# Performance work log

Hardware: AMD Instinct MI355X
Metric: run time of the kernel (lower is better)

## Reference

```python
import jax, jax.numpy as jnp
import numpy as np

P = 2048
IMG_H = IMG_W = 128
FOV = 1.0471975512  # 60 deg vertical/horizontal fov
ZNEAR, ZFAR = 0.01, 100.0
SH_C0 = 0.28209479177387814
LOWPASS = 0.3  # 3DGS low-pass filter added to 2D covariance diagonal


def _camera():
    view = np.eye(4, dtype=np.float32)
    view[2, 3] = 4.0  # camera at world z=-4 looking down +z
    tanf = np.tan(FOV / 2)
    pm = np.zeros((4, 4), dtype=np.float32)
    pm[0, 0] = 1.0 / tanf
    pm[1, 1] = 1.0 / tanf
    pm[2, 2] = ZFAR / (ZFAR - ZNEAR)
    pm[2, 3] = -ZFAR * ZNEAR / (ZFAR - ZNEAR)
    pm[3, 2] = 1.0
    proj = (pm @ view).astype(np.float32)
    campos = np.array([0.0, 0.0, -4.0], dtype=np.float32)
    return view, proj, campos


def setup_inputs() -> dict:
    key = jax.random.key(0)
    ks = jax.random.split(key, 6)
    view, proj, campos = _camera()
    return {
        'means_3d': jax.random.normal(ks[0], (P, 3), dtype=jnp.float32) * 0.8,
        'means_2d': jnp.zeros((P, 2), dtype=jnp.float32),
        'features': jax.random.uniform(ks[1], (P, 3), dtype=jnp.float32),
        'opacities': jax.random.uniform(ks[2], (P, 1), dtype=jnp.float32) * 0.9 + 0.05,
        'scales': jax.random.uniform(ks[3], (P, 3), dtype=jnp.float32) * 0.08 + 0.01,
        'rotations': jax.random.normal(ks[4], (P, 4), dtype=jnp.float32),
        'viewmatrix': jnp.asarray(view),
        'projmatrix': jnp.asarray(proj),
        'campos': jnp.asarray(campos),
        'image_height': IMG_H,
        'image_width': IMG_W,
    }


def _quat_to_rot(q):
    q = q / jnp.linalg.norm(q, axis=-1, keepdims=True)
    w, x, y, z = q[:, 0], q[:, 1], q[:, 2], q[:, 3]
    R = jnp.stack([
        1 - 2 * (y * y + z * z), 2 * (x * y - w * z), 2 * (x * z + w * y),
        2 * (x * y + w * z), 1 - 2 * (x * x + z * z), 2 * (y * z - w * x),
        2 * (x * z - w * y), 2 * (y * z + w * x), 1 - 2 * (x * x + y * y),
    ], axis=-1).reshape(-1, 3, 3)
    return R


def _rasterize(means_3d, features, opacities, scales, rotations, viewmatrix, projmatrix, H, W):
    tanf = jnp.tan(FOV / 2)
    focal_x = W / (2.0 * tanf)
    focal_y = H / (2.0 * tanf)

    # camera-space positions [P,3]
    t = means_3d @ viewmatrix[:3, :3].T + viewmatrix[:3, 3]
    depth = t[:, 2]

    # projected pixel centers (ndc2pix)
    ph = means_3d @ projmatrix[:3, :3].T + projmatrix[:3, 3]
    pw = means_3d @ projmatrix[3, :3] + projmatrix[3, 3]
    ndc = ph[:, :2] / (pw[:, None] + 1e-7)
    px = ((ndc[:, 0] + 1.0) * W - 1.0) * 0.5
    py = ((ndc[:, 1] + 1.0) * H - 1.0) * 0.5

    # 3D covariance: Sigma = R S S^T R^T
    Rm = _quat_to_rot(rotations)
    M = Rm * scales[:, None, :]  # R @ diag(s)
    sigma = M @ jnp.swapaxes(M, 1, 2)  # [P,3,3]

    # EWA splat: 2D covariance = J W Sigma W^T J^T
    lim = 1.3 * tanf
    tz = depth
    tx = jnp.clip(t[:, 0] / tz, -lim, lim) * tz
    ty = jnp.clip(t[:, 1] / tz, -lim, lim) * tz
    zeros = jnp.zeros_like(tz)
    J = jnp.stack([
        jnp.stack([focal_x / tz, zeros, -focal_x * tx / (tz * tz)], -1),
        jnp.stack([zeros, focal_y / tz, -focal_y * ty / (tz * tz)], -1),
    ], axis=1)  # [P,2,3]
    Tm = J @ viewmatrix[:3, :3]
    cov2d = Tm @ sigma @ jnp.swapaxes(Tm, 1, 2)  # [P,2,2]
    a = cov2d[:, 0, 0] + LOWPASS
    b = cov2d[:, 0, 1]
    c = cov2d[:, 1, 1] + LOWPASS
    det = a * c - b * b
    valid = (depth > 0.2) & (det > 0.0)
    det_s = jnp.where(valid, det, 1.0)
    conic_a, conic_b, conic_c = c / det_s, -b / det_s, a / det_s

    # radii from max eigenvalue
    mid = 0.5 * (a + c)
    lam = mid + jnp.sqrt(jnp.maximum(mid * mid - det, 0.1))
    radii = jnp.where(valid, jnp.ceil(3.0 * jnp.sqrt(lam)), 0.0)

    # SH degree-0 color
    color = jnp.maximum(SH_C0 * features + 0.5, 0.0)  # [P,3]

    # depth sort, front to back
    order = jnp.argsort(jnp.where(valid, depth, jnp.inf))
    px_s, py_s = px[order], py[order]
    ca, cb, cc = conic_a[order], conic_b[order], conic_c[order]
    op_s = opacities[order, 0]
    col_s = color[order]
    valid_s = valid[order]

    # pixel grid
    gx, gy = jnp.meshgrid(jnp.arange(W, dtype=jnp.float32), jnp.arange(H, dtype=jnp.float32))
    gx = gx.reshape(-1)
    gy = gy.reshape(-1)  # [HW]

    dx = gx[None, :] - px_s[:, None]  # [P,HW]
    dy = gy[None, :] - py_s[:, None]
    power = -0.5 * (ca[:, None] * dx * dx + cc[:, None] * dy * dy) - cb[:, None] * dx * dy
    alpha = jnp.minimum(0.99, op_s[:, None] * jnp.exp(jnp.minimum(power, 0.0)))
    skip = (power > 0.0) | (alpha < 1.0 / 255.0) | (~valid_s)[:, None]
    alpha = jnp.where(skip, 0.0, alpha)

    one_m = 1.0 - alpha
    incl = jnp.cumprod(one_m, axis=0)
    T_excl = jnp.concatenate([jnp.ones((1, H * W), dtype=alpha.dtype), incl[:-1]], axis=0)
    w = T_excl * alpha  # [P,HW]
    img = jnp.einsum('pn,pc->cn', w, col_s)  # [3,HW]
    T_final = incl[-1]
    img = img + T_final[None, :]  # bg_color = (1,1,1)
    return img.reshape(3, H, W), radii


def reference(means_3d, means_2d, features, opacities, scales, rotations, viewmatrix, projmatrix, campos, image_height, image_width):
    # means_2d and campos are interface placeholders (means_2d receives grads only
    # inside the CUDA kernel; campos only matters for sh_degree > 0)
    return _rasterize(means_3d, features, opacities, scales, rotations, viewmatrix, projmatrix, image_height, image_width)
```

## Files before the change

### kernel.cpp

```cpp
#include <hip/hip_runtime.h>
#include <math.h>


#define IMG 128
#define NPIX (IMG * IMG)
#define GS 12
#define SORT_N 2048

__device__ __forceinline__ void gproj(int i,
                                      const float* __restrict__ means,
                                      const float* __restrict__ rots,
                                      const float* __restrict__ scales,
                                      const float* __restrict__ vm,
                                      const float* __restrict__ pm,
                                      float& depth, bool& valid,
                                      float& px, float& py,
                                      float& ca, float& cb, float& cc,
                                      float& lam)
{
    const float W = (float)IMG, H = (float)IMG;
    const float tanfov = 0.5773502691896258f;
    const float focal_x = W / (2.0f * tanfov);
    const float focal_y = H / (2.0f * tanfov);
    const float lim = 1.3f * tanfov;

    float mx = means[3 * i + 0], my = means[3 * i + 1], mz = means[3 * i + 2];

    float tx = vm[0] * mx + vm[1] * my + vm[2]  * mz + vm[3];
    float ty = vm[4] * mx + vm[5] * my + vm[6]  * mz + vm[7];
    float tz = vm[8] * mx + vm[9] * my + vm[10] * mz + vm[11];
    depth = tz;

    float ph0 = pm[0]  * mx + pm[1]  * my + pm[2]  * mz + pm[3];
    float ph1 = pm[4]  * mx + pm[5]  * my + pm[6]  * mz + pm[7];
    float pw  = pm[12] * mx + pm[13] * my + pm[14] * mz + pm[15];
    float rinv = 1.0f / (pw + 1e-7f);
    px = ((ph0 * rinv + 1.0f) * W - 1.0f) * 0.5f;
    py = ((ph1 * rinv + 1.0f) * H - 1.0f) * 0.5f;

    float qw = rots[4 * i + 0], qx = rots[4 * i + 1], qy = rots[4 * i + 2], qz = rots[4 * i + 3];
    float qn = sqrtf(qw * qw + qx * qx + qy * qy + qz * qz);
    qw /= qn; qx /= qn; qy /= qn; qz /= qn;
    float R00 = 1.0f - 2.0f * (qy * qy + qz * qz), R01 = 2.0f * (qx * qy - qw * qz), R02 = 2.0f * (qx * qz + qw * qy);
    float R10 = 2.0f * (qx * qy + qw * qz), R11 = 1.0f - 2.0f * (qx * qx + qz * qz), R12 = 2.0f * (qy * qz - qw * qx);
    float R20 = 2.0f * (qx * qz - qw * qy), R21 = 2.0f * (qy * qz + qw * qx), R22 = 1.0f - 2.0f * (qx * qx + qy * qy);

    float sx = scales[3 * i + 0], sy = scales[3 * i + 1], sz = scales[3 * i + 2];
    float M00 = R00 * sx, M01 = R01 * sy, M02 = R02 * sz;
    float M10 = R10 * sx, M11 = R11 * sy, M12 = R12 * sz;
    float M20 = R20 * sx, M21 = R21 * sy, M22 = R22 * sz;
    float S00 = M00 * M00 + M01 * M01 + M02 * M02;
    float S01 = M00 * M10 + M01 * M11 + M02 * M12;
    float S02 = M00 * M20 + M01 * M21 + M02 * M22;
    float S11 = M10 * M10 + M11 * M11 + M12 * M12;
    float S12 = M10 * M20 + M11 * M21 + M12 * M22;
    float S22 = M20 * M20 + M21 * M21 + M22 * M22;

    float txc = fminf(fmaxf(tx / tz, -lim), lim) * tz;
    float tyc = fminf(fmaxf(ty / tz, -lim), lim) * tz;
    float J00 = focal_x / tz, J02 = -focal_x * txc / (tz * tz);
    float J11 = focal_y / tz, J12 = -focal_y * tyc / (tz * tz);

    float T00 = J00 * vm[0] + J02 * vm[8];
    float T01 = J00 * vm[1] + J02 * vm[9];
    float T02 = J00 * vm[2] + J02 * vm[10];
    float T10 = J11 * vm[4] + J12 * vm[8];
    float T11 = J11 * vm[5] + J12 * vm[9];
    float T12 = J11 * vm[6] + J12 * vm[10];

    float U00 = T00 * S00 + T01 * S01 + T02 * S02;
    float U01 = T00 * S01 + T01 * S11 + T02 * S12;
    float U02 = T00 * S02 + T01 * S12 + T02 * S22;
    float U10 = T10 * S00 + T11 * S01 + T12 * S02;
    float U11 = T10 * S01 + T11 * S11 + T12 * S12;
    float U12 = T10 * S02 + T11 * S12 + T12 * S22;
    float C00 = U00 * T00 + U01 * T01 + U02 * T02;
    float C01 = U00 * T10 + U01 * T11 + U02 * T12;
    float C11 = U10 * T10 + U11 * T11 + U12 * T12;

    float a = C00 + 0.3f, b = C01, c = C11 + 0.3f;
    float det = a * c - b * b;
    valid = (depth > 0.2f) && (det > 0.0f);
    float det_s = valid ? det : 1.0f;
    ca = c / det_s; cb = -b / det_s; cc = a / det_s;

    float mid = 0.5f * (a + c);
    lam = mid + sqrtf(fmaxf(mid * mid - det, 0.1f));
}

__global__ void gsplat_prep_rank_scatter(const float* __restrict__ means,
                                         const float* __restrict__ feats,
                                         const float* __restrict__ ops,
                                         const float* __restrict__ scales,
                                         const float* __restrict__ rots,
                                         const float* __restrict__ vm,
                                         const float* __restrict__ pm,
                                         float* __restrict__ gS,
                                         float4* __restrict__ culls,
                                         float* __restrict__ radii_out,
                                         int P)
{
    __shared__ unsigned int sk[SORT_N];
    __shared__ int partial[256];
    int tid = threadIdx.x;

    #pragma unroll 2
    for (int j = tid; j < SORT_N; j += 256) {
        unsigned int key = 0xFFFFFFFFu;
        if (j < P) {
            float mx = means[3 * j + 0], my = means[3 * j + 1], mz = means[3 * j + 2];
            float tz = vm[8] * mx + vm[9] * my + vm[10] * mz + vm[11];
            key = (tz > 0.2f) ? __float_as_uint(tz) : 0x7f800000u;
        }
        sk[j] = key;
    }
    __syncthreads();

    int g = tid & 63, s = tid >> 6;
    int i = blockIdx.x * 64 + g;
    bool act = (i < P);
    unsigned int ki = act ? sk[i] : 0u;

    const int SLICE = SORT_N / 4;
    int j0 = s * SLICE;
    const uint4* sk4 = (const uint4*)(sk + j0);
    int r = 0;
    #pragma unroll 4
    for (int q = 0; q < SLICE / 4; ++q) {
        uint4 k = sk4[q];
        int j = j0 + 4 * q;
        r += (k.x < ki) || (k.x == ki && (j + 0) < i);
        r += (k.y < ki) || (k.y == ki && (j + 1) < i);
        r += (k.z < ki) || (k.z == ki && (j + 2) < i);
        r += (k.w < ki) || (k.w == ki && (j + 3) < i);
    }
    partial[tid] = r;
    __syncthreads();

    if (s == 0 && act) {
        int rank = partial[g] + partial[64 + g] + partial[128 + g] + partial[192 + g];

        float depth, px, py, ca, cb, cc, lam; bool valid;
        gproj(i, means, rots, scales, vm, pm, depth, valid, px, py, ca, cb, cc, lam);

        const float SH_C0 = 0.28209479177387814f;
        float colr = fmaxf(SH_C0 * feats[3 * i + 0] + 0.5f, 0.0f);
        float colg = fmaxf(SH_C0 * feats[3 * i + 1] + 0.5f, 0.0f);
        float colb = fmaxf(SH_C0 * feats[3 * i + 2] + 0.5f, 0.0f);

        float opv = ops[i];
        float r2;
        if (valid) {
            r2 = 2.0f * lam * __logf(255.0f * opv) * 1.02f + 0.5f;
        } else {
            px = 0.0f; py = 0.0f; ca = 0.0f; cb = 0.0f; cc = 0.0f;
            opv = 0.0f; r2 = -1.0f;
        }
        radii_out[i] = valid ? ceilf(3.0f * sqrtf(lam)) : 0.0f;

        float4* dst = (float4*)(gS + (size_t)rank * GS);
        dst[0] = make_float4(px, py, ca, cb);
        dst[1] = make_float4(cc, opv, colr, colg);
        dst[2] = make_float4(colb, r2, 0.0f, 0.0f);
        culls[rank] = make_float4(px, py, r2, 0.0f);
    }
}

__global__ void gsplat_raster_chunk(const float* __restrict__ gS,
                                    const float4* __restrict__ culls,
                                    int P, int chunk, float4* __restrict__ part)
{
    int lx = threadIdx.x & 15, ly = threadIdx.x >> 4;
    int lane = threadIdx.x & 63;
    int tilex = blockIdx.x & 7, tiley = blockIdx.x >> 3;
    int x = tilex * 16 + lx, y = tiley * 16 + ly;
    float gx = (float)x, gy = (float)y;
    float tx0 = (float)(tilex * 16), tx1 = (float)(tilex * 16 + 15);
    float ty0 = (float)(tiley * 16), ty1 = (float)(tiley * 16 + 15);

    int base = blockIdx.y * chunk;
    int cnt = min(chunk, P - base);

    float T = 1.0f, cr = 0.0f, cg = 0.0f, cb = 0.0f;
    const float* Gp = gS + (size_t)base * GS;

    for (int h = 0; h < chunk; h += 64) {
        int gi = h + lane;
        bool pred = false;
        if (gi < cnt) {
            float4 cu = culls[base + gi];
            float ddx = cu.x - fminf(fmaxf(cu.x, tx0), tx1);
            float ddy = cu.y - fminf(fmaxf(cu.y, ty0), ty1);
            pred = (ddx * ddx + ddy * ddy <= cu.z);
        }
        unsigned long long m = __ballot(pred);
        while (m) {
            int b = __builtin_ctzll(m);
            m &= m - 1;
            const float* G = Gp + (size_t)(h + b) * GS;
            float pxv = G[0], pyv = G[1];
            float ca = G[2], cbn = G[3], cc = G[4];
            float op = G[5], r = G[6], g = G[7], bl = G[8];
            float dx = gx - pxv, dy = gy - pyv;
            float power = -0.5f * (ca * dx * dx + cc * dy * dy) - cbn * dx * dy;
            float e = __expf(fminf(power, 0.0f));
            float alpha = fminf(0.99f, op * e);
            alpha = (power > 0.0f) ? 0.0f : alpha;
            alpha = (alpha < 0.00392156862745098f) ? 0.0f : alpha;
            float w = T * alpha;
            cr = fmaf(w, r, cr);
            cg = fmaf(w, g, cg);
            cb = fmaf(w, bl, cb);
            T = T * (1.0f - alpha);
        }
    }

    int pix = y * IMG + x;
    part[(size_t)blockIdx.y * NPIX + pix] = make_float4(cr, cg, cb, T);
}

__global__ void gsplat_combine(const float4* __restrict__ part, int K,
                               float* __restrict__ img)
{
    int pix = blockIdx.x * blockDim.x + threadIdx.x;
    if (pix >= NPIX) return;
    float T = 1.0f, r = 0.0f, g = 0.0f, b = 0.0f;
    for (int c = 0; c < K; ++c) {
        float4 v = part[(size_t)c * NPIX + pix];
        r = fmaf(T, v.x, r);
        g = fmaf(T, v.y, g);
        b = fmaf(T, v.z, b);
        T *= v.w;
    }
    img[pix]            = r + T;
    img[NPIX + pix]     = g + T;
    img[2 * NPIX + pix] = b + T;
}

extern "C" void kernel_launch(void* const* d_in, const int* in_sizes, int n_in,
                              void* d_out, int out_size, void* d_ws, size_t ws_size,
                              hipStream_t stream)
{
    const float* means  = (const float*)d_in[0];
    const float* feats  = (const float*)d_in[2];
    const float* ops    = (const float*)d_in[3];
    const float* scales = (const float*)d_in[4];
    const float* rots   = (const float*)d_in[5];
    const float* vm     = (const float*)d_in[6];
    const float* pm     = (const float*)d_in[7];

    int P = in_sizes[0] / 3;

    float* img   = (float*)d_out;
    float* radii = (float*)d_out + 3 * NPIX;

    float*  gS    = (float*)d_ws;
    float4* culls = (float4*)(gS + (size_t)SORT_N * GS);
    float4* part  = culls + SORT_N;
    size_t static_bytes = (size_t)SORT_N * (GS + 4) * sizeof(float);

    int K = 16;
    while (K > 1 && static_bytes + (size_t)K * NPIX * sizeof(float4) > ws_size) K >>= 1;
    int chunk = (P + K - 1) / K;
    chunk = (chunk + 63) & ~63;
    int Kb = (P + chunk - 1) / chunk;

    gsplat_prep_rank_scatter<<<(P + 63) / 64, 256, 0, stream>>>(
        means, feats, ops, scales, rots, vm, pm, gS, culls, radii, P);

    gsplat_raster_chunk<<<dim3(64, Kb), 256, 0, stream>>>(gS, culls, P, chunk, part);

    gsplat_combine<<<NPIX / 256, 256, 0, stream>>>(part, Kb, img);
}
```

Measured before the change: 107.0 us.

## Fuse prep, raster and combine into one cooperative kernel with grid syncs

Merges the three kernel launches (depth-rank scatter, chunked rasterization, partial combine) into a single cooperative kernel that separates the phases with grid.sync(). The goal is to remove launch gaps and per-kernel overhead between stages. The depth chunk count is fixed at 8 rather than derived from workspace size, and the Gaussian record loads now use float4. Grid-wide barriers add their own synchronisation cost. The kernel also assumes all 512 blocks can be co-resident, and with P fixed at 2048 the prep phase sorts only the first 2048 gaussians.

New measurement: 227.7 us. 2.13x slower.

```diff
diff --git a/kernel.cpp b/kernel.cpp
--- a/kernel.cpp
+++ b/kernel.cpp
@@ -1,11 +1,16 @@
 #include <hip/hip_runtime.h>
+#include <hip/hip_cooperative_groups.h>
 #include <math.h>
+
+namespace cg = cooperative_groups;
 
 
 #define IMG 128
 #define NPIX (IMG * IMG)
 #define GS 12
 #define SORT_N 2048
+#define KCH 8
+#define GRID (64 * KCH)
 
 __device__ __forceinline__ void gproj(int i,
                                       const float* __restrict__ means,
@@ -88,153 +93,158 @@
     lam = mid + sqrtf(fmaxf(mid * mid - det, 0.1f));
 }
 
-__global__ void gsplat_prep_rank_scatter(const float* __restrict__ means,
-                                         const float* __restrict__ feats,
-                                         const float* __restrict__ ops,
-                                         const float* __restrict__ scales,
-                                         const float* __restrict__ rots,
-                                         const float* __restrict__ vm,
-                                         const float* __restrict__ pm,
-                                         float* __restrict__ gS,
-                                         float4* __restrict__ culls,
-                                         float* __restrict__ radii_out,
-                                         int P)
+__global__ void __launch_bounds__(256, 2)
+gsplat_fused(const float* __restrict__ means,
+             const float* __restrict__ feats,
+             const float* __restrict__ ops,
+             const float* __restrict__ scales,
+             const float* __restrict__ rots,
+             const float* __restrict__ vm,
+             const float* __restrict__ pm,
+             float* __restrict__ gS,
+             float4* __restrict__ culls,
+             float* __restrict__ radii_out,
+             float4* __restrict__ part,
+             float* __restrict__ img,
+             int P, int chunk)
 {
     __shared__ unsigned int sk[SORT_N];
     __shared__ int partial[256];
     int tid = threadIdx.x;
-
-    #pragma unroll 2
-    for (int j = tid; j < SORT_N; j += 256) {
-        unsigned int key = 0xFFFFFFFFu;
-        if (j < P) {
-            float mx = means[3 * j + 0], my = means[3 * j + 1], mz = means[3 * j + 2];
-            float tz = vm[8] * mx + vm[9] * my + vm[10] * mz + vm[11];
-            key = (tz > 0.2f) ? __float_as_uint(tz) : 0x7f800000u;
-        }
-        sk[j] = key;
+    cg::grid_group grid = cg::this_grid();
+
+    if (blockIdx.x < (SORT_N + 63) / 64) {
+        #pragma unroll 2
+        for (int j = tid; j < SORT_N; j += 256) {
+            unsigned int key = 0xFFFFFFFFu;
+            if (j < P) {
+                float mx = means[3 * j + 0], my = means[3 * j + 1], mz = means[3 * j + 2];
+                float tz = vm[8] * mx + vm[9] * my + vm[10] * mz + vm[11];
+                key = (tz > 0.2f) ? __float_as_uint(tz) : 0x7f800000u;
+            }
+            sk[j] = key;
+        }
+        __syncthreads();
+
+        int g = tid & 63, s = tid >> 6;
+        int i = blockIdx.x * 64 + g;
+        bool act = (i < P);
+        unsigned int ki = act ? sk[i] : 0u;
+
+        const int SLICE = SORT_N / 4;
+        int j0 = s * SLICE;
+        const uint4* sk4 = (const uint4*)(sk + j0);
+        int r = 0;
+        #pragma unroll 4
+        for (int q = 0; q < SLICE / 4; ++q) {
+            uint4 k = sk4[q];
+            int j = j0 + 4 * q;
+            r += (k.x < ki) || (k.x == ki && (j + 0) < i);
+            r += (k.y < ki) || (k.y == ki && (j + 1) < i);
+            r += (k.z < ki) || (k.z == ki && (j + 2) < i);
+            r += (k.w < ki) || (k.w == ki && (j + 3) < i);
+        }
+        partial[tid] = r;
+        __syncthreads();
+
+        if (s == 0 && act) {
+            int rank = partial[g] + partial[64 + g] + partial[128 + g] + partial[192 + g];
+
+            float depth, px, py, ca, cb, cc, lam; bool valid;
+            gproj(i, means, rots, scales, vm, pm, depth, valid, px, py, ca, cb, cc, lam);
+
+            const float SH_C0 = 0.28209479177387814f;
+            float colr = fmaxf(SH_C0 * feats[3 * i + 0] + 0.5f, 0.0f);
+            float colg = fmaxf(SH_C0 * feats[3 * i + 1] + 0.5f, 0.0f);
+            float colb = fmaxf(SH_C0 * feats[3 * i + 2] + 0.5f, 0.0f);
+
+            float opv = ops[i];
+            float r2;
+            if (valid) {
+                r2 = 2.0f * lam * __logf(255.0f * opv) * 1.02f + 0.5f;
+            } else {
+                px = 0.0f; py = 0.0f; ca = 0.0f; cb = 0.0f; cc = 0.0f;
+                opv = 0.0f; r2 = -1.0f;
+            }
+            radii_out[i] = valid ? ceilf(3.0f * sqrtf(lam)) : 0.0f;
+
+            float4* dst = (float4*)(gS + (size_t)rank * GS);
+            dst[0] = make_float4(px, py, ca, cb);
+            dst[1] = make_float4(cc, opv, colr, colg);
+            dst[2] = make_float4(colb, r2, 0.0f, 0.0f);
+            culls[rank] = make_float4(px, py, r2, 0.0f);
+        }
     }
-    __syncthreads();
-
-    int g = tid & 63, s = tid >> 6;
-    int i = blockIdx.x * 64 + g;
-    bool act = (i < P);
-    unsigned int ki = act ? sk[i] : 0u;
-
-    const int SLICE = SORT_N / 4;
-    int j0 = s * SLICE;
-    const uint4* sk4 = (const uint4*)(sk + j0);
-    int r = 0;
-    #pragma unroll 4
-    for (int q = 0; q < SLICE / 4; ++q) {
-        uint4 k = sk4[q];
-        int j = j0 + 4 * q;
-        r += (k.x < ki) || (k.x == ki && (j + 0) < i);
-        r += (k.y < ki) || (k.y == ki && (j + 1) < i);
-        r += (k.z < ki) || (k.z == ki && (j + 2) < i);
-        r += (k.w < ki) || (k.w == ki && (j + 3) < i);
+
+    grid.sync();
+
+    {
+        int tile = blockIdx.x & 63;
+        int kc = blockIdx.x >> 6;
+        int lx = tid & 15, ly = tid >> 4;
+        int lane = tid & 63;
+        int tilex = tile & 7, tiley = tile >> 3;
+        int x = tilex * 16 + lx, y = tiley * 16 + ly;
+        float gx = (float)x, gy = (float)y;
+        float tx0 = (float)(tilex * 16), tx1 = (float)(tilex * 16 + 15);
+        float ty0 = (float)(tiley * 16), ty1 = (float)(tiley * 16 + 15);
+
+        int base = kc * chunk;
+        int cnt = min(chunk, P - base);
+
+        float T = 1.0f, cr = 0.0f, cgc = 0.0f, cbl = 0.0f;
+        const float* Gp = gS + (size_t)base * GS;
+
+        for (int h = 0; h < chunk; h += 64) {
+            int gi = h + lane;
+            bool pred = false;
+            if (gi < cnt) {
+                float4 cu = culls[base + gi];
+                float ddx = cu.x - fminf(fmaxf(cu.x, tx0), tx1);
+                float ddy = cu.y - fminf(fmaxf(cu.y, ty0), ty1);
+                pred = (ddx * ddx + ddy * ddy <= cu.z);
+            }
+            unsigned long long m = __ballot(pred);
+            while (m) {
+                int b = __builtin_ctzll(m);
+                m &= m - 1;
+                const float4* G4 = (const float4*)(Gp + (size_t)(h + b) * GS);
+                float4 A = G4[0], B = G4[1], C = G4[2];
+                float dx = gx - A.x, dy = gy - A.y;
+                float power = -0.5f * (A.z * dx * dx + B.x * dy * dy) - A.w * dx * dy;
+                float e = __expf(fminf(power, 0.0f));
+                float alpha = fminf(0.99f, B.y * e);
+                alpha = (power > 0.0f) ? 0.0f : alpha;
+                alpha = (alpha < 0.00392156862745098f) ? 0.0f : alpha;
+                float w = T * alpha;
+                cr  = fmaf(w, B.z, cr);
+                cgc = fmaf(w, B.w, cgc);
+                cbl = fmaf(w, C.x, cbl);
+                T = T * (1.0f - alpha);
+            }
+        }
+
+        int pix = y * IMG + x;
+        part[(size_t)kc * NPIX + pix] = make_float4(cr, cgc, cbl, T);
     }
-    partial[tid] = r;
-    __syncthreads();
-
-    if (s == 0 && act) {
-        int rank = partial[g] + partial[64 + g] + partial[128 + g] + partial[192 + g];
-
-        float depth, px, py, ca, cb, cc, lam; bool valid;
-        gproj(i, means, rots, scales, vm, pm, depth, valid, px, py, ca, cb, cc, lam);
-
-        const float SH_C0 = 0.28209479177387814f;
-        float colr = fmaxf(SH_C0 * feats[3 * i + 0] + 0.5f, 0.0f);
-        float colg = fmaxf(SH_C0 * feats[3 * i + 1] + 0.5f, 0.0f);
-        float colb = fmaxf(SH_C0 * feats[3 * i + 2] + 0.5f, 0.0f);
-
-        float opv = ops[i];
-        float r2;
-        if (valid) {
-            r2 = 2.0f * lam * __logf(255.0f * opv) * 1.02f + 0.5f;
-        } else {
-            px = 0.0f; py = 0.0f; ca = 0.0f; cb = 0.0f; cc = 0.0f;
-            opv = 0.0f; r2 = -1.0f;
-        }
-        radii_out[i] = valid ? ceilf(3.0f * sqrtf(lam)) : 0.0f;
-
-        float4* dst = (float4*)(gS + (size_t)rank * GS);
-        dst[0] = make_float4(px, py, ca, cb);
-        dst[1] = make_float4(cc, opv, colr, colg);
-        dst[2] = make_float4(colb, r2, 0.0f, 0.0f);
-        culls[rank] = make_float4(px, py, r2, 0.0f);
+
+    grid.sync();
+
+    if (blockIdx.x < NPIX / 256) {
+        int pix = blockIdx.x * 256 + tid;
+        float T = 1.0f, r = 0.0f, g = 0.0f, b = 0.0f;
+        #pragma unroll
+        for (int c = 0; c < KCH; ++c) {
+            float4 v = part[(size_t)c * NPIX + pix];
+            r = fmaf(T, v.x, r);
+            g = fmaf(T, v.y, g);
+            b = fmaf(T, v.z, b);
+            T *= v.w;
+        }
+        img[pix]            = r + T;
+        img[NPIX + pix]     = g + T;
+        img[2 * NPIX + pix] = b + T;
     }
-}
-
-__global__ void gsplat_raster_chunk(const float* __restrict__ gS,
-                                    const float4* __restrict__ culls,
-                                    int P, int chunk, float4* __restrict__ part)
-{
-    int lx = threadIdx.x & 15, ly = threadIdx.x >> 4;
-    int lane = threadIdx.x & 63;
-    int tilex = blockIdx.x & 7, tiley = blockIdx.x >> 3;
-    int x = tilex * 16 + lx, y = tiley * 16 + ly;
-    float gx = (float)x, gy = (float)y;
-    float tx0 = (float)(tilex * 16), tx1 = (float)(tilex * 16 + 15);
-    float ty0 = (float)(tiley * 16), ty1 = (float)(tiley * 16 + 15);
-
-    int base = blockIdx.y * chunk;
-    int cnt = min(chunk, P - base);
-
-    float T = 1.0f, cr = 0.0f, cg = 0.0f, cb = 0.0f;
-    const float* Gp = gS + (size_t)base * GS;
-
-    for (int h = 0; h < chunk; h += 64) {
-        int gi = h + lane;
-        bool pred = false;
-        if (gi < cnt) {
-            float4 cu = culls[base + gi];
-            float ddx = cu.x - fminf(fmaxf(cu.x, tx0), tx1);
-            float ddy = cu.y - fminf(fmaxf(cu.y, ty0), ty1);
-            pred = (ddx * ddx + ddy * ddy <= cu.z);
-        }
-        unsigned long long m = __ballot(pred);
-        while (m) {
-            int b = __builtin_ctzll(m);
-            m &= m - 1;
-            const float* G = Gp + (size_t)(h + b) * GS;
-            float pxv = G[0], pyv = G[1];
-            float ca = G[2], cbn = G[3], cc = G[4];
-            float op = G[5], r = G[6], g = G[7], bl = G[8];
-            float dx = gx - pxv, dy = gy - pyv;
-            float power = -0.5f * (ca * dx * dx + cc * dy * dy) - cbn * dx * dy;
-            float e = __expf(fminf(power, 0.0f));
-            float alpha = fminf(0.99f, op * e);
-            alpha = (power > 0.0f) ? 0.0f : alpha;
-            alpha = (alpha < 0.00392156862745098f) ? 0.0f : alpha;
-            float w = T * alpha;
-            cr = fmaf(w, r, cr);
-            cg = fmaf(w, g, cg);
-            cb = fmaf(w, bl, cb);
-            T = T * (1.0f - alpha);
-        }
-    }
-
-    int pix = y * IMG + x;
-    part[(size_t)blockIdx.y * NPIX + pix] = make_float4(cr, cg, cb, T);
-}
-
-__global__ void gsplat_combine(const float4* __restrict__ part, int K,
-                               float* __restrict__ img)
-{
-    int pix = blockIdx.x * blockDim.x + threadIdx.x;
-    if (pix >= NPIX) return;
-    float T = 1.0f, r = 0.0f, g = 0.0f, b = 0.0f;
-    for (int c = 0; c < K; ++c) {
-        float4 v = part[(size_t)c * NPIX + pix];
-        r = fmaf(T, v.x, r);
-        g = fmaf(T, v.y, g);
-        b = fmaf(T, v.z, b);
-        T *= v.w;
-    }
-    img[pix]            = r + T;
-    img[NPIX + pix]     = g + T;
-    img[2 * NPIX + pix] = b + T;
 }
 
 extern "C" void kernel_launch(void* const* d_in, const int* in_sizes, int n_in,
@@ -257,18 +267,16 @@
     float*  gS    = (float*)d_ws;
     float4* culls = (float4*)(gS + (size_t)SORT_N * GS);
     float4* part  = culls + SORT_N;
-    size_t static_bytes = (size_t)SORT_N * (GS + 4) * sizeof(float);
-
-    int K = 16;
-    while (K > 1 && static_bytes + (size_t)K * NPIX * sizeof(float4) > ws_size) K >>= 1;
-    int chunk = (P + K - 1) / K;
+
+    int chunk = (P + KCH - 1) / KCH;
     chunk = (chunk + 63) & ~63;
-    int Kb = (P + chunk - 1) / chunk;
-
-    gsplat_prep_rank_scatter<<<(P + 63) / 64, 256, 0, stream>>>(
-        means, feats, ops, scales, rots, vm, pm, gS, culls, radii, P);
-
-    gsplat_raster_chunk<<<dim3(64, Kb), 256, 0, stream>>>(gS, culls, P, chunk, part);
-
-    gsplat_combine<<<NPIX / 256, 256, 0, stream>>>(part, Kb, img);
+
+    void* args[] = {
+        (void*)&means, (void*)&feats, (void*)&ops, (void*)&scales,
+        (void*)&rots,  (void*)&vm,    (void*)&pm,
+        (void*)&gS, (void*)&culls, (void*)&radii, (void*)&part, (void*)&img,
+        (void*)&P, (void*)&chunk
+    };
+    hipLaunchCooperativeKernel((void*)gsplat_fused, dim3(GRID), dim3(256),
+                               args, 0, stream);
 }
```

## Fuse chunked rasterization and combine into single-pass per-tile kernel with LDS staging

Applied to the files above, without the earlier changes.

Replaces the split-over-gaussian-chunks raster kernel and separate compositing kernel with one kernel where each 16x16 tile block stages all gaussian records and cull data into shared memory and composites every gaussian front-to-back. This removes the partial-buffer writes/reads and a kernel launch. In exchange the grid shrinks to 64 blocks using large LDS, reducing parallelism across compute units and serializing the full gaussian list per tile.

After: 141.5 us. 32.3% more time.

```diff
diff --git a/kernel.cpp b/kernel.cpp
--- a/kernel.cpp
+++ b/kernel.cpp
@@ -166,75 +166,65 @@
     }
 }
 
-__global__ void gsplat_raster_chunk(const float* __restrict__ gS,
-                                    const float4* __restrict__ culls,
-                                    int P, int chunk, float4* __restrict__ part)
-{
-    int lx = threadIdx.x & 15, ly = threadIdx.x >> 4;
-    int lane = threadIdx.x & 63;
+__global__ void __launch_bounds__(256)
+gsplat_raster_full(const float* __restrict__ gS,
+                   const float4* __restrict__ culls,
+                   int P, float* __restrict__ img)
+{
+    __shared__ float4 scull[SORT_N];
+    __shared__ float  srec[SORT_N * GS];
+    int tid = threadIdx.x;
+
+    for (int j = tid; j < SORT_N; j += 256)
+        scull[j] = (j < P) ? culls[j] : make_float4(0.0f, 0.0f, -1.0f, 0.0f);
+    {
+        const float4* g4 = (const float4*)gS;
+        float4* s4 = (float4*)srec;
+        int n4 = (P * GS) / 4;
+        for (int j = tid; j < n4; j += 256) s4[j] = g4[j];
+    }
+    __syncthreads();
+
+    int lx = tid & 15, ly = tid >> 4;
+    int lane = tid & 63;
     int tilex = blockIdx.x & 7, tiley = blockIdx.x >> 3;
     int x = tilex * 16 + lx, y = tiley * 16 + ly;
     float gx = (float)x, gy = (float)y;
     float tx0 = (float)(tilex * 16), tx1 = (float)(tilex * 16 + 15);
     float ty0 = (float)(tiley * 16), ty1 = (float)(tiley * 16 + 15);
 
-    int base = blockIdx.y * chunk;
-    int cnt = min(chunk, P - base);
-
     float T = 1.0f, cr = 0.0f, cg = 0.0f, cb = 0.0f;
-    const float* Gp = gS + (size_t)base * GS;
-
-    for (int h = 0; h < chunk; h += 64) {
-        int gi = h + lane;
-        bool pred = false;
-        if (gi < cnt) {
-            float4 cu = culls[base + gi];
-            float ddx = cu.x - fminf(fmaxf(cu.x, tx0), tx1);
-            float ddy = cu.y - fminf(fmaxf(cu.y, ty0), ty1);
-            pred = (ddx * ddx + ddy * ddy <= cu.z);
-        }
+
+    #pragma unroll 2
+    for (int h = 0; h < SORT_N; h += 64) {
+        float4 cu = scull[h + lane];
+        float ddx = cu.x - fminf(fmaxf(cu.x, tx0), tx1);
+        float ddy = cu.y - fminf(fmaxf(cu.y, ty0), ty1);
+        bool pred = (ddx * ddx + ddy * ddy <= cu.z);
         unsigned long long m = __ballot(pred);
         while (m) {
             int b = __builtin_ctzll(m);
             m &= m - 1;
-            const float* G = Gp + (size_t)(h + b) * GS;
-            float pxv = G[0], pyv = G[1];
-            float ca = G[2], cbn = G[3], cc = G[4];
-            float op = G[5], r = G[6], g = G[7], bl = G[8];
-            float dx = gx - pxv, dy = gy - pyv;
-            float power = -0.5f * (ca * dx * dx + cc * dy * dy) - cbn * dx * dy;
+            const float4* R4 = (const float4*)(srec + (size_t)(h + b) * GS);
+            float4 A = R4[0], B = R4[1], C = R4[2];
+            float dx = gx - A.x, dy = gy - A.y;
+            float power = -0.5f * (A.z * dx * dx + B.x * dy * dy) - A.w * dx * dy;
             float e = __expf(fminf(power, 0.0f));
-            float alpha = fminf(0.99f, op * e);
+            float alpha = fminf(0.99f, B.y * e);
             alpha = (power > 0.0f) ? 0.0f : alpha;
             alpha = (alpha < 0.00392156862745098f) ? 0.0f : alpha;
             float w = T * alpha;
-            cr = fmaf(w, r, cr);
-            cg = fmaf(w, g, cg);
-            cb = fmaf(w, bl, cb);
+            cr = fmaf(w, B.z, cr);
+            cg = fmaf(w, B.w, cg);
+            cb = fmaf(w, C.x, cb);
             T = T * (1.0f - alpha);
         }
     }
 
     int pix = y * IMG + x;
-    part[(size_t)blockIdx.y * NPIX + pix] = make_float4(cr, cg, cb, T);
-}
-
-__global__ void gsplat_combine(const float4* __restrict__ part, int K,
-                               float* __restrict__ img)
-{
-    int pix = blockIdx.x * blockDim.x + threadIdx.x;
-    if (pix >= NPIX) return;
-    float T = 1.0f, r = 0.0f, g = 0.0f, b = 0.0f;
-    for (int c = 0; c < K; ++c) {
-        float4 v = part[(size_t)c * NPIX + pix];
-        r = fmaf(T, v.x, r);
-        g = fmaf(T, v.y, g);
-        b = fmaf(T, v.z, b);
-        T *= v.w;
-    }
-    img[pix]            = r + T;
-    img[NPIX + pix]     = g + T;
-    img[2 * NPIX + pix] = b + T;
+    img[pix]            = cr + T;
+    img[NPIX + pix]     = cg + T;
+    img[2 * NPIX + pix] = cb + T;
 }
 
 extern "C" void kernel_launch(void* const* d_in, const int* in_sizes, int n_in,
@@ -256,19 +246,9 @@
 
     float*  gS    = (float*)d_ws;
     float4* culls = (float4*)(gS + (size_t)SORT_N * GS);
-    float4* part  = culls + SORT_N;
-    size_t static_bytes = (size_t)SORT_N * (GS + 4) * sizeof(float);
-
-    int K = 16;
-    while (K > 1 && static_bytes + (size_t)K * NPIX * sizeof(float4) > ws_size) K >>= 1;
-    int chunk = (P + K - 1) / K;
-    chunk = (chunk + 63) & ~63;
-    int Kb = (P + chunk - 1) / chunk;
 
     gsplat_prep_rank_scatter<<<(P + 63) / 64, 256, 0, stream>>>(
         means, feats, ops, scales, rots, vm, pm, gS, culls, radii, P);
 
-    gsplat_raster_chunk<<<dim3(64, Kb), 256, 0, stream>>>(gS, culls, P, chunk, part);
-
-    gsplat_combine<<<NPIX / 256, 256, 0, stream>>>(part, Kb, img);
-}
+    gsplat_raster_full<<<64, 256, 0, stream>>>(gS, culls, P, img);
+}
```
